# Performance work log

Measured on AMD Instinct MI355X. Metric: run time of the kernel, lower is better.

The kernel has to match this reference:

```python
import jax, jax.numpy as jnp
import numpy as np

BN_EPS = 1e-5

def _resize_hw(x, hw):
    # bilinear per temporal slice (align_corners=False == jax half-pixel 'linear');
    # T dim keeps its size so linear resize is identity along it.
    B, C, T, H, W = x.shape
    return jax.image.resize(x, (B, C, T, hw, hw), method='linear')

def setup_inputs() -> dict:
    key = jax.random.key(0)
    ks = jax.random.split(key, 12)
    Cin, Cmid = 80, 40
    s = lambda k, shp, scale=0.05: jax.random.normal(k, shp, dtype=jnp.float32) * scale
    return {
        'fast': jax.random.normal(ks[0], (1, Cin, 4, 64, 64), dtype=jnp.float32),
        'slow': jax.random.normal(ks[1], (1, Cin, 4, 64, 64), dtype=jnp.float32),
        'g_w': s(ks[2], (Cmid, Cin)), 'g_b': s(ks[3], (Cmid,)),
        'th_w': s(ks[4], (Cmid, Cin)), 'th_b': s(ks[5], (Cmid,)),
        'ph_w': s(ks[6], (Cmid, Cin)), 'ph_b': s(ks[7], (Cmid,)),
        'wz_w': s(ks[8], (Cin, Cmid)), 'wz_b': s(ks[9], (Cin,)),
        'bn_g': 1.0 + s(ks[10], (Cin,)), 'bn_b': s(ks[11], (Cin,)),
    }

def reference(fast, slow, g_w, g_b, th_w, th_b, ph_w, ph_b, wz_w, wz_b, bn_g, bn_b):
    x_fast = _resize_hw(fast, 32)   # [B,80,4,32,32]
    x_slow = _resize_hw(slow, 32)
    B, C, T, H, W = x_fast.shape
    N = T * H * W
    flat = x_fast.reshape(B, C, N)                      # [B,C,N]
    # 1x1 conv projections (channel contractions)
    g_x = jnp.einsum('oc,bcn->bno', g_w, flat) + g_b          # [B,N,Cm]
    theta = jnp.einsum('oc,bcn->bno', th_w, flat) + th_b      # [B,N,Cm]
    phi = jnp.einsum('oc,bcn->bon', ph_w, flat) + ph_b[None, :, None]  # [B,Cm,N]
    f = jnp.einsum('bnc,bcm->bnm', theta, phi)          # [B,N,N] full attention scores
    f_div_C = jax.nn.softmax(f, axis=-1)                # 'embedded' mode
    y = jnp.einsum('bnm,bmc->bnc', f_div_C, g_x)        # [B,N,Cm]
    y = y.transpose(0, 2, 1).reshape(B, -1, T, H, W)    # [B,Cm,T,H,W]
    # W_z: 1x1 conv then training-mode BatchNorm3d (batch stats over N,T,H,W)
    wy = jnp.einsum('oc,bcthw->bothw', wz_w, y) + wz_b[None, :, None, None, None]
    mean = jnp.mean(wy, axis=(0, 2, 3, 4), keepdims=True)
    var = jnp.var(wy, axis=(0, 2, 3, 4), keepdims=True)
    gamma = bn_g[None, :, None, None, None]
    beta = bn_b[None, :, None, None, None]
    wy = (wy - mean) * jax.lax.rsqrt(var + BN_EPS) * gamma + beta
    z = wy * x_slow                                     # elementwise fast/slow fusion
    return _resize_hw(z, 64)                            # [B,80,4,64,64]
```

## Files before the change

kernel.cpp:

```cpp
#include <hip/hip_runtime.h>

typedef unsigned int u32;
typedef __bf16 bf16x8 __attribute__((ext_vector_type(8)));
typedef float f32x4 __attribute__((ext_vector_type(4)));
typedef u32 u32x4 __attribute__((ext_vector_type(4)));


static __device__ __forceinline__ u32 f2bf(float f) {
    u32 u = __float_as_uint(f);
    return (u + 0x7fffu + ((u >> 16) & 1u)) >> 16;
}

__device__ __forceinline__ void taps_down(int i, int* j, float* w) {
    if (i == 0) {
        j[0]=0; j[1]=0; j[2]=1; j[3]=2;
        w[0]=0.f; w[1]=3.f/7.f; w[2]=3.f/7.f; w[3]=1.f/7.f;
    } else if (i == 31) {
        j[0]=61; j[1]=62; j[2]=63; j[3]=63;
        w[0]=1.f/7.f; w[1]=3.f/7.f; w[2]=3.f/7.f; w[3]=0.f;
    } else {
        j[0]=2*i-1; j[1]=2*i; j[2]=2*i+1; j[3]=2*i+2;
        w[0]=0.125f; w[1]=0.375f; w[2]=0.375f; w[3]=0.125f;
    }
}

__global__ __launch_bounds__(256) void k_down(
        const float* __restrict__ fast, const float* __restrict__ slow,
        float* __restrict__ xf, float* __restrict__ xs) {
    int idx = blockIdx.x * 256 + threadIdx.x;
    int which = idx >= 327680;
    int rem = which ? idx - 327680 : idx;
    const float* src = which ? slow : fast;
    float* dst = which ? xs : xf;
    int c = rem >> 12;
    int n = rem & 4095;
    int tt = n >> 10, hh = (n >> 5) & 31, ww = n & 31;
    int jy[4], jx[4]; float wy[4], wx[4];
    taps_down(hh, jy, wy);
    taps_down(ww, jx, wx);
    const float* base = src + ((c * 4 + tt) << 12);
    float acc = 0.f;
#pragma unroll
    for (int a = 0; a < 4; ++a) {
        const float* row = base + (jy[a] << 6);
        acc += wy[a] * (wx[0]*row[jx[0]] + wx[1]*row[jx[1]]
                      + wx[2]*row[jx[2]] + wx[3]*row[jx[3]]);
    }
    dst[rem] = acc;
}

__global__ __launch_bounds__(256) void k_proj(
        const float* __restrict__ xf,
        const float* __restrict__ gw, const float* __restrict__ gb,
        const float* __restrict__ thw, const float* __restrict__ thb,
        const float* __restrict__ phw, const float* __restrict__ phb,
        unsigned short* __restrict__ gxP, unsigned short* __restrict__ thetaP,
        unsigned short* __restrict__ phiP) {
    __shared__ float sW[480];
    __shared__ float sB[6];
    int t = threadIdx.x;
    int o0 = blockIdx.y * 2;
    for (int i = t; i < 480; i += 256) {
        int mat = i / 160, rem = i % 160;
        int oo = rem / 80, c = rem % 80;
        const float* w = (mat == 0) ? gw : ((mat == 1) ? thw : phw);
        sW[i] = w[(o0 + oo) * 80 + c];
    }
    if (t < 6) {
        int mat = t / 2, oo = t % 2;
        const float* b = (mat == 0) ? gb : ((mat == 1) ? thb : phb);
        sB[t] = b[o0 + oo];
    }
    __syncthreads();
    int n = blockIdx.x * 256 + t;
    if (blockIdx.y == 0) {
#pragma unroll
        for (int c = 40; c < 64; ++c) { thetaP[n*64 + c] = 0; phiP[n*64 + c] = 0; }
#pragma unroll
        for (int r = 40; r < 48; ++r) gxP[r * 4096 + n] = 0;
    }
    float x[80];
#pragma unroll
    for (int c = 0; c < 80; ++c) x[c] = xf[c * 4096 + n];
#pragma unroll
    for (int mat = 0; mat < 3; ++mat) {
#pragma unroll
        for (int oo = 0; oo < 2; ++oo) {
            float acc = sB[mat * 2 + oo];
            const float4* w4 = (const float4*)&sW[mat * 160 + oo * 80];
#pragma unroll
            for (int cq = 0; cq < 20; ++cq) {
                float4 w = w4[cq];
                acc += w.x * x[cq*4] + w.y * x[cq*4+1] + w.z * x[cq*4+2] + w.w * x[cq*4+3];
            }
            int o = o0 + oo;
            if (mat == 0)      gxP[o * 4096 + n]  = (unsigned short)f2bf(acc);
            else if (mat == 1) thetaP[n * 64 + o] = (unsigned short)f2bf(acc);
            else               phiP[n * 64 + o]   = (unsigned short)f2bf(acc);
        }
    }
}

#define YMM(acc, gfr, bfr) \
    acc = __builtin_amdgcn_mfma_f32_16x16x32_bf16( \
        __builtin_bit_cast(bf16x8, gfr), __builtin_bit_cast(bf16x8, bfr), acc, 0, 0, 0)

__global__ __launch_bounds__(256) void k_attn(
        const unsigned short* __restrict__ thetaP,
        const unsigned short* __restrict__ phiP,
        const unsigned short* __restrict__ gxP,
        float* __restrict__ yfin) {
    __shared__ float yred[4][48][16];
    __shared__ float sred[4][16];
    int t = threadIdx.x;
    int lane = t & 63;
    int wv = t >> 6;
    int n0 = blockIdx.x * 16;
    int nl = lane & 15, q = lane >> 4;

    const unsigned short* thp = thetaP + (n0 + nl) * 64 + q * 8;
    u32x4 tb0 = *(const u32x4*)(thp);
    u32x4 tb1 = *(const u32x4*)(thp + 32);

    f32x4 y0 = {0.f,0.f,0.f,0.f}, y1 = y0, y2 = y0;
    float ssum = 0.f;
    int idx0 = ((((q & 1) << 5) + nl) << 2);
    int idx1 = idx0 + 64;

    u32x4 pfA[4], pfB[4], gfA[3], gfB[3];
    int mbase = wv * 1024;

#define LOADBLK(P, G, BLK) do {                                              \
        int m0_ = mbase + (BLK) * 32;                                        \
        const unsigned short* pp0_ = phiP + (m0_ + nl) * 64 + q * 8;         \
        const unsigned short* pp1_ = phiP + (m0_ + 16 + nl) * 64 + q * 8;    \
        P[0] = *(const u32x4*)pp0_;  P[1] = *(const u32x4*)(pp0_ + 32);      \
        P[2] = *(const u32x4*)pp1_;  P[3] = *(const u32x4*)(pp1_ + 32);      \
        G[0] = *(const u32x4*)(gxP + (nl) * 4096      + m0_ + q * 8);        \
        G[1] = *(const u32x4*)(gxP + (16 + nl) * 4096 + m0_ + q * 8);        \
        G[2] = *(const u32x4*)(gxP + (32 + nl) * 4096 + m0_ + q * 8);        \
    } while (0)

#define COMPUTE(P, G) do {                                                   \
        u32 p0[2], p1[2];                                                    \
        _Pragma("unroll")                                                    \
        for (int Tm = 0; Tm < 2; ++Tm) {                                     \
            f32x4 f = {0.f,0.f,0.f,0.f};                                     \
            f = __builtin_amdgcn_mfma_f32_16x16x32_bf16(                     \
                __builtin_bit_cast(bf16x8, P[Tm*2+0]),                       \
                __builtin_bit_cast(bf16x8, tb0), f, 0, 0, 0);                \
            f = __builtin_amdgcn_mfma_f32_16x16x32_bf16(                     \
                __builtin_bit_cast(bf16x8, P[Tm*2+1]),                       \
                __builtin_bit_cast(bf16x8, tb1), f, 0, 0, 0);                \
            float e0 = __expf(f[0]), e1 = __expf(f[1]);                      \
            float e2 = __expf(f[2]), e3 = __expf(f[3]);                      \
            ssum += (e0 + e1) + (e2 + e3);                                   \
            p0[Tm] = f2bf(e0) | (f2bf(e1) << 16);                            \
            p1[Tm] = f2bf(e2) | (f2bf(e3) << 16);                            \
        }                                                                    \
        int a0 = __builtin_amdgcn_ds_bpermute(idx0, (int)p0[0]);             \
        int a1 = __builtin_amdgcn_ds_bpermute(idx0, (int)p1[0]);             \
        int a2 = __builtin_amdgcn_ds_bpermute(idx1, (int)p0[0]);             \
        int a3 = __builtin_amdgcn_ds_bpermute(idx1, (int)p1[0]);             \
        int b0 = __builtin_amdgcn_ds_bpermute(idx0, (int)p0[1]);             \
        int b1 = __builtin_amdgcn_ds_bpermute(idx0, (int)p1[1]);             \
        int b2 = __builtin_amdgcn_ds_bpermute(idx1, (int)p0[1]);             \
        int b3 = __builtin_amdgcn_ds_bpermute(idx1, (int)p1[1]);             \
        u32x4 bf_;                                                           \
        bf_[0] = (u32)(q < 2 ? a0 : b0);  bf_[1] = (u32)(q < 2 ? a1 : b1);   \
        bf_[2] = (u32)(q < 2 ? a2 : b2);  bf_[3] = (u32)(q < 2 ? a3 : b3);   \
        YMM(y0, G[0], bf_);  YMM(y1, G[1], bf_);  YMM(y2, G[2], bf_);        \
    } while (0)

    LOADBLK(pfA, gfA, 0);
#pragma unroll 1
    for (int bb = 0; bb < 16; ++bb) {
        LOADBLK(pfB, gfB, bb * 2 + 1);
        COMPUTE(pfA, gfA);
        if (bb < 15) LOADBLK(pfA, gfA, bb * 2 + 2);
        COMPUTE(pfB, gfB);
    }

    ssum += __shfl_xor(ssum, 16);
    ssum += __shfl_xor(ssum, 32);
    if (lane < 16) sred[wv][lane] = ssum;
#pragma unroll
    for (int r = 0; r < 4; ++r) {
        yred[wv][q * 4 + r][nl]      = y0[r];
        yred[wv][16 + q * 4 + r][nl] = y1[r];
        yred[wv][32 + q * 4 + r][nl] = y2[r];
    }
    __syncthreads();

    for (int v = t; v < 768; v += 256) {
        int c = v >> 4, n = v & 15;
        if (c < 40) {
            float s  = (yred[0][c][n] + yred[1][c][n])
                     + (yred[2][c][n] + yred[3][c][n]);
            float ss = (sred[0][n] + sred[1][n]) + (sred[2][n] + sred[3][n]);
            yfin[c * 4096 + n0 + n] = s / ss;
        }
    }
}

__device__ __forceinline__ void taps_up(int i, int* j0, int* j1, float* w0, float* w1) {
    if (i == 0)        { *j0 = 0;        *j1 = 0;          *w0 = 0.f;   *w1 = 1.f;   }
    else if (i == 63)  { *j0 = 31;       *j1 = 31;         *w0 = 1.f;   *w1 = 0.f;   }
    else if (i & 1)    { *j0 = i >> 1;   *j1 = (i>>1) + 1; *w0 = 0.75f; *w1 = 0.25f; }
    else               { *j0 = (i>>1)-1; *j1 = i >> 1;     *w0 = 0.25f; *w1 = 0.75f; }
}

__global__ __launch_bounds__(256) void k_bn_up(
        const float* __restrict__ yfin, const float* __restrict__ wzw,
        const float* __restrict__ wzb, const float* __restrict__ bng,
        const float* __restrict__ bnb, const float* __restrict__ xs,
        float* __restrict__ out) {
    __shared__ float4 wrow4[1024];
    __shared__ float sred[8];
    int ch = blockIdx.x;
    int t = threadIdx.x;
    float w[40];
#pragma unroll
    for (int o = 0; o < 40; ++o) w[o] = wzw[ch * 40 + o];
    float bias = wzb[ch];
    float s1 = 0.f, s2 = 0.f;
#pragma unroll 1
    for (int k = 0; k < 4; ++k) {
        int i = k * 256 + t;
        float4 yv[40];
#pragma unroll
        for (int o = 0; o < 40; ++o)
            yv[o] = *(const float4*)(yfin + o * 4096 + i * 4);
        float4 a = make_float4(bias, bias, bias, bias);
#pragma unroll
        for (int o = 0; o < 40; ++o) {
            a.x += w[o]*yv[o].x; a.y += w[o]*yv[o].y;
            a.z += w[o]*yv[o].z; a.w += w[o]*yv[o].w;
        }
        wrow4[i] = a;
        s1 += a.x + a.y + a.z + a.w;
        s2 += a.x*a.x + a.y*a.y + a.z*a.z + a.w*a.w;
    }
#pragma unroll
    for (int off = 32; off > 0; off >>= 1) {
        s1 += __shfl_down(s1, off);
        s2 += __shfl_down(s2, off);
    }
    int wid = t >> 6;
    if ((t & 63) == 0) { sred[wid] = s1; sred[4 + wid] = s2; }
    __syncthreads();
    float mean = (sred[0] + sred[1] + sred[2] + sred[3]) * (1.f / 4096.f);
    float var  = (sred[4] + sred[5] + sred[6] + sred[7]) * (1.f / 4096.f) - mean * mean;
    float inv = rsqrtf(var + 1e-5f);
    float sc = bng[ch] * inv;
    float sh = bnb[ch] - mean * sc;
#pragma unroll
    for (int k = 0; k < 4; ++k) {
        int i = k * 256 + t;
        float4 a = wrow4[i];
        float4 xv = *(const float4*)(xs + ch * 4096 + i * 4);
        a.x = (a.x*sc + sh)*xv.x; a.y = (a.y*sc + sh)*xv.y;
        a.z = (a.z*sc + sh)*xv.z; a.w = (a.w*sc + sh)*xv.w;
        wrow4[i] = a;
    }
    __syncthreads();
    const float* zs = (const float*)wrow4;
    int chbase = ch << 14;
#pragma unroll 4
    for (int k = 0; k < 64; ++k) {
        int p = k * 256 + t;
        int tt = p >> 12, yy = (p >> 6) & 63, xx = p & 63;
        int jy0, jy1, jx0, jx1; float wy0, wy1, wx0, wx1;
        taps_up(yy, &jy0, &jy1, &wy0, &wy1);
        taps_up(xx, &jx0, &jx1, &wx0, &wx1);
        const float* pl = zs + tt * 1024;
        float r0 = wx0*pl[jy0*32 + jx0] + wx1*pl[jy0*32 + jx1];
        float r1 = wx0*pl[jy1*32 + jx0] + wx1*pl[jy1*32 + jx1];
        out[chbase + p] = wy0*r0 + wy1*r1;
    }
}

extern "C" void kernel_launch(void* const* d_in, const int* in_sizes, int n_in,
                              void* d_out, int out_size, void* d_ws, size_t ws_size,
                              hipStream_t stream) {
    const float* fast = (const float*)d_in[0];
    const float* slow = (const float*)d_in[1];
    const float* g_w  = (const float*)d_in[2];
    const float* g_b  = (const float*)d_in[3];
    const float* th_w = (const float*)d_in[4];
    const float* th_b = (const float*)d_in[5];
    const float* ph_w = (const float*)d_in[6];
    const float* ph_b = (const float*)d_in[7];
    const float* wz_w = (const float*)d_in[8];
    const float* wz_b = (const float*)d_in[9];
    const float* bn_g = (const float*)d_in[10];
    const float* bn_b = (const float*)d_in[11];
    float* out = (float*)d_out;
    float* ws  = (float*)d_ws;

    float* xf = ws;
    float* xs = ws + 327680;
    unsigned short* thetaP = (unsigned short*)(ws + 655360);
    unsigned short* phiP   = (unsigned short*)(ws + 786432);
    unsigned short* gxP    = (unsigned short*)(ws + 917504);
    float* yfin  = ws + 1015808;

    k_down<<<2560, 256, 0, stream>>>(fast, slow, xf, xs);
    k_proj<<<dim3(16, 20), 256, 0, stream>>>(xf, g_w, g_b, th_w, th_b, ph_w, ph_b,
                                             gxP, thetaP, phiP);
    k_attn<<<256, 256, 0, stream>>>(thetaP, phiP, gxP, yfin);
    k_bn_up<<<80, 256, 0, stream>>>(yfin, wz_w, wz_b, bn_g, bn_b, xs, out);
}
```

Measured before the change: 140.6 us.

## Split attention keys across blocks, widen query tile, fuse slow downsample into BN

Each attention block now handles 32 query rows instead of 16, reusing every loaded phi/g fragment for two query tiles. The key range is split across two blocks (grid y=2), which write unnormalized partial outputs and partial softmax sums. The softmax normalization and the sum over the two partials move into the BN/upsample kernel. The slow-input downsample also moves there, done from an LDS-staged plane, which removes half of k_down and the xs round trip. The trade-off is more work and about 96KB of LDS in the 80-block BN kernel, which may lengthen that serial stage.

```diff
diff --git a/kernel.cpp b/kernel.cpp
--- a/kernel.cpp
+++ b/kernel.cpp
@@ -25,20 +25,15 @@
 }
 
 __global__ __launch_bounds__(256) void k_down(
-        const float* __restrict__ fast, const float* __restrict__ slow,
-        float* __restrict__ xf, float* __restrict__ xs) {
-    int idx = blockIdx.x * 256 + threadIdx.x;
-    int which = idx >= 327680;
-    int rem = which ? idx - 327680 : idx;
-    const float* src = which ? slow : fast;
-    float* dst = which ? xs : xf;
+        const float* __restrict__ fast, float* __restrict__ xf) {
+    int rem = blockIdx.x * 256 + threadIdx.x;
     int c = rem >> 12;
     int n = rem & 4095;
     int tt = n >> 10, hh = (n >> 5) & 31, ww = n & 31;
     int jy[4], jx[4]; float wy[4], wx[4];
     taps_down(hh, jy, wy);
     taps_down(ww, jx, wx);
-    const float* base = src + ((c * 4 + tt) << 12);
+    const float* base = fast + ((c * 4 + tt) << 12);
     float acc = 0.f;
 #pragma unroll
     for (int a = 0; a < 4; ++a) {
@@ -46,7 +41,7 @@
         acc += wy[a] * (wx[0]*row[jx[0]] + wx[1]*row[jx[1]]
                       + wx[2]*row[jx[2]] + wx[3]*row[jx[3]]);
     }
-    dst[rem] = acc;
+    xf[rem] = acc;
 }
 
 __global__ __launch_bounds__(256) void k_proj(
@@ -109,26 +104,32 @@
         const unsigned short* __restrict__ thetaP,
         const unsigned short* __restrict__ phiP,
         const unsigned short* __restrict__ gxP,
-        float* __restrict__ yfin) {
-    __shared__ float yred[4][48][16];
-    __shared__ float sred[4][16];
+        float* __restrict__ ypart, float* __restrict__ spart) {
+    __shared__ float yred[4][48][32];
+    __shared__ float sred[4][32];
     int t = threadIdx.x;
     int lane = t & 63;
     int wv = t >> 6;
-    int n0 = blockIdx.x * 16;
+    int i = blockIdx.x;
+    int j = blockIdx.y;
+    int n0 = i * 32;
     int nl = lane & 15, q = lane >> 4;
 
-    const unsigned short* thp = thetaP + (n0 + nl) * 64 + q * 8;
-    u32x4 tb0 = *(const u32x4*)(thp);
-    u32x4 tb1 = *(const u32x4*)(thp + 32);
-
-    f32x4 y0 = {0.f,0.f,0.f,0.f}, y1 = y0, y2 = y0;
-    float ssum = 0.f;
+    const unsigned short* thpa = thetaP + (n0 + nl) * 64 + q * 8;
+    const unsigned short* thpb = thetaP + (n0 + 16 + nl) * 64 + q * 8;
+    u32x4 tba0 = *(const u32x4*)(thpa);
+    u32x4 tba1 = *(const u32x4*)(thpa + 32);
+    u32x4 tbb0 = *(const u32x4*)(thpb);
+    u32x4 tbb1 = *(const u32x4*)(thpb + 32);
+
+    f32x4 ya0 = {0.f,0.f,0.f,0.f}, ya1 = ya0, ya2 = ya0;
+    f32x4 yb0 = ya0, yb1 = ya0, yb2 = ya0;
+    float ssa = 0.f, ssb = 0.f;
     int idx0 = ((((q & 1) << 5) + nl) << 2);
     int idx1 = idx0 + 64;
 
     u32x4 pfA[4], pfB[4], gfA[3], gfB[3];
-    int mbase = wv * 1024;
+    int mbase = j * 2048 + wv * 512;
 
 #define LOADBLK(P, G, BLK) do {                                              \
         int m0_ = mbase + (BLK) * 32;                                        \
@@ -141,20 +142,20 @@
         G[2] = *(const u32x4*)(gxP + (32 + nl) * 4096 + m0_ + q * 8);        \
     } while (0)
 
-#define COMPUTE(P, G) do {                                                   \
+#define NT_COMPUTE(P, G, TB0, TB1, Y0, Y1, Y2, SS) do {                      \
         u32 p0[2], p1[2];                                                    \
         _Pragma("unroll")                                                    \
         for (int Tm = 0; Tm < 2; ++Tm) {                                     \
             f32x4 f = {0.f,0.f,0.f,0.f};                                     \
             f = __builtin_amdgcn_mfma_f32_16x16x32_bf16(                     \
                 __builtin_bit_cast(bf16x8, P[Tm*2+0]),                       \
-                __builtin_bit_cast(bf16x8, tb0), f, 0, 0, 0);                \
+                __builtin_bit_cast(bf16x8, TB0), f, 0, 0, 0);                \
             f = __builtin_amdgcn_mfma_f32_16x16x32_bf16(                     \
                 __builtin_bit_cast(bf16x8, P[Tm*2+1]),                       \
-                __builtin_bit_cast(bf16x8, tb1), f, 0, 0, 0);                \
+                __builtin_bit_cast(bf16x8, TB1), f, 0, 0, 0);                \
             float e0 = __expf(f[0]), e1 = __expf(f[1]);                      \
             float e2 = __expf(f[2]), e3 = __expf(f[3]);                      \
-            ssum += (e0 + e1) + (e2 + e3);                                   \
+            SS += (e0 + e1) + (e2 + e3);                                     \
             p0[Tm] = f2bf(e0) | (f2bf(e1) << 16);                            \
             p1[Tm] = f2bf(e2) | (f2bf(e3) << 16);                            \
         }                                                                    \
@@ -169,37 +170,48 @@
         u32x4 bf_;                                                           \
         bf_[0] = (u32)(q < 2 ? a0 : b0);  bf_[1] = (u32)(q < 2 ? a1 : b1);   \
         bf_[2] = (u32)(q < 2 ? a2 : b2);  bf_[3] = (u32)(q < 2 ? a3 : b3);   \
-        YMM(y0, G[0], bf_);  YMM(y1, G[1], bf_);  YMM(y2, G[2], bf_);        \
+        YMM(Y0, G[0], bf_);  YMM(Y1, G[1], bf_);  YMM(Y2, G[2], bf_);        \
+    } while (0)
+
+#define COMPUTE(P, G) do {                                                   \
+        NT_COMPUTE(P, G, tba0, tba1, ya0, ya1, ya2, ssa);                    \
+        NT_COMPUTE(P, G, tbb0, tbb1, yb0, yb1, yb2, ssb);                    \
     } while (0)
 
     LOADBLK(pfA, gfA, 0);
 #pragma unroll 1
-    for (int bb = 0; bb < 16; ++bb) {
+    for (int bb = 0; bb < 8; ++bb) {
         LOADBLK(pfB, gfB, bb * 2 + 1);
         COMPUTE(pfA, gfA);
-        if (bb < 15) LOADBLK(pfA, gfA, bb * 2 + 2);
+        if (bb < 7) LOADBLK(pfA, gfA, bb * 2 + 2);
         COMPUTE(pfB, gfB);
     }
 
-    ssum += __shfl_xor(ssum, 16);
-    ssum += __shfl_xor(ssum, 32);
-    if (lane < 16) sred[wv][lane] = ssum;
+    ssa += __shfl_xor(ssa, 16);  ssa += __shfl_xor(ssa, 32);
+    ssb += __shfl_xor(ssb, 16);  ssb += __shfl_xor(ssb, 32);
+    if (lane < 16) { sred[wv][lane] = ssa; sred[wv][16 + lane] = ssb; }
 #pragma unroll
     for (int r = 0; r < 4; ++r) {
-        yred[wv][q * 4 + r][nl]      = y0[r];
-        yred[wv][16 + q * 4 + r][nl] = y1[r];
-        yred[wv][32 + q * 4 + r][nl] = y2[r];
-    }
-    __syncthreads();
-
-    for (int v = t; v < 768; v += 256) {
-        int c = v >> 4, n = v & 15;
+        yred[wv][q * 4 + r][nl]           = ya0[r];
+        yred[wv][16 + q * 4 + r][nl]      = ya1[r];
+        yred[wv][32 + q * 4 + r][nl]      = ya2[r];
+        yred[wv][q * 4 + r][16 + nl]      = yb0[r];
+        yred[wv][16 + q * 4 + r][16 + nl] = yb1[r];
+        yred[wv][32 + q * 4 + r][16 + nl] = yb2[r];
+    }
+    __syncthreads();
+
+    for (int v = t; v < 1536; v += 256) {
+        int c = v >> 5, nn = v & 31;
         if (c < 40) {
-            float s  = (yred[0][c][n] + yred[1][c][n])
-                     + (yred[2][c][n] + yred[3][c][n]);
-            float ss = (sred[0][n] + sred[1][n]) + (sred[2][n] + sred[3][n]);
-            yfin[c * 4096 + n0 + n] = s / ss;
+            float s = (yred[0][c][nn] + yred[1][c][nn])
+                    + (yred[2][c][nn] + yred[3][c][nn]);
+            ypart[j * 163840 + c * 4096 + n0 + nn] = s;
         }
+    }
+    if (t < 32) {
+        float s = (sred[0][t] + sred[1][t]) + (sred[2][t] + sred[3][t]);
+        spart[j * 4096 + n0 + t] = s;
     }
 }
 
@@ -211,14 +223,40 @@
 }
 
 __global__ __launch_bounds__(256) void k_bn_up(
-        const float* __restrict__ yfin, const float* __restrict__ wzw,
-        const float* __restrict__ wzb, const float* __restrict__ bng,
-        const float* __restrict__ bnb, const float* __restrict__ xs,
-        float* __restrict__ out) {
+        const float* __restrict__ ypart, const float* __restrict__ spart,
+        const float* __restrict__ wzw, const float* __restrict__ wzb,
+        const float* __restrict__ bng, const float* __restrict__ bnb,
+        const float* __restrict__ slow, float* __restrict__ out) {
+    __shared__ float splane[16384];
+    __shared__ float dsx[4096];
     __shared__ float4 wrow4[1024];
-    __shared__ float sred[8];
+    __shared__ float sredl[8];
     int ch = blockIdx.x;
     int t = threadIdx.x;
+
+    const float4* sp4 = (const float4*)(slow + (ch << 14));
+    float4* spl4 = (float4*)splane;
+#pragma unroll
+    for (int k = 0; k < 16; ++k) spl4[k * 256 + t] = sp4[k * 256 + t];
+    __syncthreads();
+#pragma unroll 1
+    for (int k = 0; k < 16; ++k) {
+        int n = k * 256 + t;
+        int tt = n >> 10, hh = (n >> 5) & 31, ww = n & 31;
+        int jy[4], jx[4]; float wy[4], wx[4];
+        taps_down(hh, jy, wy);
+        taps_down(ww, jx, wx);
+        const float* base = splane + (tt << 12);
+        float acc = 0.f;
+#pragma unroll
+        for (int a = 0; a < 4; ++a) {
+            const float* row = base + (jy[a] << 6);
+            acc += wy[a] * (wx[0]*row[jx[0]] + wx[1]*row[jx[1]]
+                          + wx[2]*row[jx[2]] + wx[3]*row[jx[3]]);
+        }
+        dsx[n] = acc;
+    }
+
     float w[40];
 #pragma unroll
     for (int o = 0; o < 40; ++o) w[o] = wzw[ch * 40 + o];
@@ -227,16 +265,31 @@
 #pragma unroll 1
     for (int k = 0; k < 4; ++k) {
         int i = k * 256 + t;
-        float4 yv[40];
-#pragma unroll
-        for (int o = 0; o < 40; ++o)
-            yv[o] = *(const float4*)(yfin + o * 4096 + i * 4);
-        float4 a = make_float4(bias, bias, bias, bias);
-#pragma unroll
-        for (int o = 0; o < 40; ++o) {
-            a.x += w[o]*yv[o].x; a.y += w[o]*yv[o].y;
-            a.z += w[o]*yv[o].z; a.w += w[o]*yv[o].w;
+        float4 sa = *(const float4*)(spart + i * 4);
+        float4 sb = *(const float4*)(spart + 4096 + i * 4);
+        float4 inv = make_float4(1.f/(sa.x+sb.x), 1.f/(sa.y+sb.y),
+                                 1.f/(sa.z+sb.z), 1.f/(sa.w+sb.w));
+        float4 raw = make_float4(0.f, 0.f, 0.f, 0.f);
+#pragma unroll 1
+        for (int half = 0; half < 2; ++half) {
+            float4 va[20], vb[20];
+#pragma unroll
+            for (int oo = 0; oo < 20; ++oo) {
+                int o = half * 20 + oo;
+                va[oo] = *(const float4*)(ypart + o * 4096 + i * 4);
+                vb[oo] = *(const float4*)(ypart + 163840 + o * 4096 + i * 4);
+            }
+#pragma unroll
+            for (int oo = 0; oo < 20; ++oo) {
+                float wo = w[half * 20 + oo];
+                raw.x += wo * (va[oo].x + vb[oo].x);
+                raw.y += wo * (va[oo].y + vb[oo].y);
+                raw.z += wo * (va[oo].z + vb[oo].z);
+                raw.w += wo * (va[oo].w + vb[oo].w);
+            }
         }
+        float4 a = make_float4(bias + raw.x*inv.x, bias + raw.y*inv.y,
+                               bias + raw.z*inv.z, bias + raw.w*inv.w);
         wrow4[i] = a;
         s1 += a.x + a.y + a.z + a.w;
         s2 += a.x*a.x + a.y*a.y + a.z*a.z + a.w*a.w;
@@ -247,10 +300,10 @@
         s2 += __shfl_down(s2, off);
     }
     int wid = t >> 6;
-    if ((t & 63) == 0) { sred[wid] = s1; sred[4 + wid] = s2; }
-    __syncthreads();
-    float mean = (sred[0] + sred[1] + sred[2] + sred[3]) * (1.f / 4096.f);
-    float var  = (sred[4] + sred[5] + sred[6] + sred[7]) * (1.f / 4096.f) - mean * mean;
+    if ((t & 63) == 0) { sredl[wid] = s1; sredl[4 + wid] = s2; }
+    __syncthreads();
+    float mean = (sredl[0] + sredl[1] + sredl[2] + sredl[3]) * (1.f / 4096.f);
+    float var  = (sredl[4] + sredl[5] + sredl[6] + sredl[7]) * (1.f / 4096.f) - mean * mean;
     float inv = rsqrtf(var + 1e-5f);
     float sc = bng[ch] * inv;
     float sh = bnb[ch] - mean * sc;
@@ -258,7 +311,7 @@
     for (int k = 0; k < 4; ++k) {
         int i = k * 256 + t;
         float4 a = wrow4[i];
-        float4 xv = *(const float4*)(xs + ch * 4096 + i * 4);
+        float4 xv = ((const float4*)dsx)[i];
         a.x = (a.x*sc + sh)*xv.x; a.y = (a.y*sc + sh)*xv.y;
         a.z = (a.z*sc + sh)*xv.z; a.w = (a.w*sc + sh)*xv.w;
         wrow4[i] = a;
@@ -299,15 +352,15 @@
     float* ws  = (float*)d_ws;
 
     float* xf = ws;
-    float* xs = ws + 327680;
-    unsigned short* thetaP = (unsigned short*)(ws + 655360);
-    unsigned short* phiP   = (unsigned short*)(ws + 786432);
-    unsigned short* gxP    = (unsigned short*)(ws + 917504);
-    float* yfin  = ws + 1015808;
-
-    k_down<<<2560, 256, 0, stream>>>(fast, slow, xf, xs);
+    unsigned short* thetaP = (unsigned short*)(ws + 327680);
+    unsigned short* phiP   = (unsigned short*)(ws + 458752);
+    unsigned short* gxP    = (unsigned short*)(ws + 589824);
+    float* ypart = ws + 688128;
+    float* spart = ws + 1015808;
+
+    k_down<<<1280, 256, 0, stream>>>(fast, xf);
     k_proj<<<dim3(16, 20), 256, 0, stream>>>(xf, g_w, g_b, th_w, th_b, ph_w, ph_b,
                                              gxP, thetaP, phiP);
-    k_attn<<<256, 256, 0, stream>>>(thetaP, phiP, gxP, yfin);
-    k_bn_up<<<80, 256, 0, stream>>>(yfin, wz_w, wz_b, bn_g, bn_b, xs, out);
-}
+    k_attn<<<dim3(128, 2), 256, 0, stream>>>(thetaP, phiP, gxP, ypart, spart);
+    k_bn_up<<<80, 256, 0, stream>>>(ypart, spart, wz_w, wz_b, bn_g, bn_b, slow, out);
+}
```

After: 145.8 us. +3.7%, slower.
